# Optimization experiments

Hardware: AMD Instinct MI355X
Metric: run time of the kernel (lower is better)

The kernel has to match this reference:

```python
import jax, jax.numpy as jnp
import numpy as np
from jax import lax

CHUNK = 64
D_CONV = 4
EPS = 1e-5


def _rmsnorm(x, w):
    ms = jnp.mean(jnp.square(x.astype(jnp.float32)), axis=-1, keepdims=True)
    return x * lax.rsqrt(ms + EPS).astype(x.dtype) * w


def _conv_mix(x, proj_w, gate_w, conv_w, conv_b, out_proj_w):
    # x: [B,L,D] -> depthwise causal conv on projected channels, silu gate, out proj
    B, L, D = x.shape
    val = jnp.einsum('bld,ed->ble', x, proj_w)            # [B,L,d_inner]
    v = val.transpose(0, 2, 1)                            # [B,d_inner,L]
    d_inner = proj_w.shape[0]
    v = lax.conv_general_dilated(
        v, conv_w, window_strides=(1,), padding=[(D_CONV - 1, 0)],
        dimension_numbers=('NCH', 'OIH', 'NCH'), feature_group_count=d_inner)
    v = v + conv_b[None, :, None]
    val = jax.nn.silu(v.transpose(0, 2, 1))               # [B,L,d_inner]
    gate = jax.nn.silu(jnp.einsum('bld,ed->ble', x, gate_w))
    return jnp.einsum('ble,de->bld', val * gate, out_proj_w)


def _memory_attend(out, write_w, read_w, decay, log_alpha):
    B, T, D = out.shape
    C = CHUNK
    out32 = out.astype(jnp.float32)
    gamma = jax.nn.sigmoid(decay)
    log_gamma = jnp.log(gamma)
    v = jnp.einsum('btd,ed->bte', out32, write_w)         # proj_write
    wk = jnp.pad(out32[:, :-1], ((0, 0), (1, 0), (0, 0)))  # shifted keys
    rk = out32
    p = jnp.arange(C, dtype=jnp.float32)
    gp = gamma ** p                                       # [C]
    gw = gamma ** (C - 1 - p)                              # [C]
    diffs = jnp.maximum(p[:, None] - 1.0 - p[None, :], 0.0)
    M = jnp.exp(diffs * log_gamma) * (p[:, None] > p[None, :])  # [C,C]
    gC = gamma ** C
    Nc = T // C
    # scan axis first: [Nc,B,C,D]
    rk_c = rk.reshape(B, Nc, C, D).transpose(1, 0, 2, 3)
    wk_c = wk.reshape(B, Nc, C, D).transpose(1, 0, 2, 3)
    v_c = v.reshape(B, Nc, C, D).transpose(1, 0, 2, 3)

    def step(W, chunk):
        r, k, vv = chunk                                  # each [B,C,D]
        inter = jnp.einsum('bcd,bed->bce', r, W) * gp[None, :, None]
        S = jnp.einsum('bcd,bed->bce', r, k)              # [B,C,C]
        intra = jnp.einsum('bce,bed->bcd', S * M, vv)
        W_new = gC * W + jnp.einsum('bcd,bce->bde', vv * gw[None, :, None], k)
        return W_new, inter + intra

    W0 = jnp.zeros((B, D, D), dtype=jnp.float32)
    _, reads = lax.scan(step, W0, (rk_c, wk_c, v_c))      # [Nc,B,C,D]
    reads = reads.transpose(1, 0, 2, 3).reshape(B, T, D)
    read_out = jnp.einsum('btd,ed->bte', reads, read_w)
    return out + jnp.exp(log_alpha) * read_out.astype(out.dtype)


def setup_inputs() -> dict:
    key = jax.random.key(0)
    ks = jax.random.split(key, 9)
    B, T, D, d_inner = 8, 4096, 768, 1536
    s_d = 1.0 / np.sqrt(D)
    s_i = 1.0 / np.sqrt(d_inner)
    return {
        'x': jax.random.normal(ks[0], (B, T, D), jnp.float32),
        'norm_w': jnp.ones((D,), jnp.float32),
        'proj_w': jax.random.normal(ks[1], (d_inner, D), jnp.float32) * s_d,
        'gate_w': jax.random.normal(ks[2], (d_inner, D), jnp.float32) * s_d,
        'conv_w': jax.random.normal(ks[3], (d_inner, 1, D_CONV), jnp.float32) * 0.5,
        'conv_b': jnp.zeros((d_inner,), jnp.float32),
        'out_proj_w': jax.random.normal(ks[4], (D, d_inner), jnp.float32) * s_i,
        'write_w': jax.random.normal(ks[5], (D, D), jnp.float32) * s_d,
        'read_w': jax.random.normal(ks[6], (D, D), jnp.float32) * s_d,
        'decay': jnp.float32(4.6),
        'log_alpha': jnp.log(jnp.float32(0.03)),
    }


def reference(x, norm_w, proj_w, gate_w, conv_w, conv_b, out_proj_w, write_w, read_w, decay, log_alpha):
    out = _conv_mix(_rmsnorm(x, norm_w), proj_w, gate_w, conv_w, conv_b, out_proj_w)
    out = _memory_attend(out, write_w, read_w, decay, log_alpha)
    return x + out
```

## Files before the change

kernel.cpp:

```cpp
#include <hip/hip_runtime.h>
#include <stdint.h>


typedef short bf16s;
typedef __attribute__((ext_vector_type(8))) short short8;
typedef __attribute__((ext_vector_type(4))) float f32x4;

#define DEVINL __device__ __forceinline__

DEVINL float bf2f(short s) {
    union { unsigned u; float f; } v; v.u = ((unsigned)(unsigned short)s) << 16; return v.f;
}
DEVINL short f2bf(float f) {
    union { float f; unsigned u; } v; v.f = f;
    unsigned r = v.u + 0x7fffu + ((v.u >> 16) & 1u);
    return (short)(r >> 16);
}

DEVINL void glds16(void* lds, const void* g) {
    __builtin_amdgcn_global_load_lds(
        (const __attribute__((address_space(1))) void*)g,
        (__attribute__((address_space(3))) void*)lds, 16, 0, 0);
}

DEVINL void stage128(bf16s* lds, const bf16s* g, long gstride, int wave) {
#pragma unroll
    for (int p = 0; p < 4; ++p)
        glds16(lds + p * 2048 + wave * 512, g + (long)p * 32 * gstride);
}

DEVINL short8 fragr(const bf16s* t, int row, int kk, int q) {
    int f = kk * 4 + q;
    return *(const short8*)(t + row * 64 + ((f ^ (row & 7)) * 8));
}

#define MFMA(a, b, c) __builtin_amdgcn_mfma_f32_16x16x32_bf16((a), (b), (c), 0, 0, 0)

__global__ __launch_bounds__(256) void cast_w_kernel(
    const float* __restrict__ proj, const float* __restrict__ gate,
    const float* __restrict__ op, const float* __restrict__ wr, const float* __restrict__ rd,
    bf16s* __restrict__ w_pg, bf16s* __restrict__ w_op, bf16s* __restrict__ w_wr,
    bf16s* __restrict__ w_rd) {
    long i = (long)blockIdx.x * 256 + threadIdx.x;
    if (i < 1179648)        w_pg[i] = f2bf(proj[i]);
    else if (i < 2359296)   w_pg[i] = f2bf(gate[i - 1179648]);
    else if (i < 3538944)   w_op[i - 2359296] = f2bf(op[i - 2359296]);
    else if (i < 4128768)   w_wr[i - 3538944] = f2bf(wr[i - 3538944]);
    else if (i < 4718592)   w_rd[i - 4128768] = f2bf(rd[i - 4128768]);
}

__global__ __launch_bounds__(256) void rmsnorm_kernel(
    const float* __restrict__ x, const float* __restrict__ w, bf16s* __restrict__ xn) {
    long row = blockIdx.x;
    const float* xr = x + row * 768;
    int tid = threadIdx.x;
    float v0 = xr[tid], v1 = xr[tid + 256], v2 = xr[tid + 512];
    float ss = v0 * v0 + v1 * v1 + v2 * v2;
#pragma unroll
    for (int off = 32; off; off >>= 1) ss += __shfl_down(ss, off);
    __shared__ float p[4];
    if ((tid & 63) == 0) p[tid >> 6] = ss;
    __syncthreads();
    float tot = p[0] + p[1] + p[2] + p[3];
    float s = rsqrtf(tot * (1.0f / 768.0f) + 1e-5f);
    bf16s* o = xn + row * 768;
    o[tid]       = f2bf(v0 * s * w[tid]);
    o[tid + 256] = f2bf(v1 * s * w[tid + 256]);
    o[tid + 512] = f2bf(v2 * s * w[tid + 512]);
}

template <int MODE>
__global__ __launch_bounds__(256, 2) void gemm_kernel(
    const bf16s* __restrict__ A, const bf16s* __restrict__ B, int K, int N,
    bf16s* __restrict__ Cb, const float* __restrict__ xres,
    const bf16s* __restrict__ outres, const float* __restrict__ p_la,
    float* __restrict__ Cout) {
    __shared__ bf16s sA[128 * 64];
    __shared__ bf16s sB[128 * 64];
    const int tid = threadIdx.x;
    const int wave = tid >> 6, lane = tid & 63;
    const int wm = wave >> 1, wn = wave & 1;
    const int ln15 = lane & 15, q = lane >> 4;
    const long m0 = (long)blockIdx.y * 128, n0 = (long)blockIdx.x * 128;
    const int sr = tid >> 3;
    const int sf = (tid & 7) ^ (sr & 7);
    const bf16s* gA = A + (m0 + sr) * K + sf * 8;
    const bf16s* gB = B + (n0 + sr) * K + sf * 8;
    f32x4 acc[4][4] = {};
    const int nkt = K >> 6;
    for (int kt = 0; kt < nkt; ++kt) {
        __syncthreads();
        stage128(sA, gA, K, wave);
        stage128(sB, gB, K, wave);
        gA += 64; gB += 64;
        asm volatile("s_waitcnt vmcnt(0)" ::: "memory");
        __syncthreads();
#pragma unroll
        for (int kk = 0; kk < 2; ++kk) {
            short8 af[4], bf_[4];
#pragma unroll
            for (int i = 0; i < 4; ++i) af[i] = fragr(sA, wm * 64 + i * 16 + ln15, kk, q);
#pragma unroll
            for (int j = 0; j < 4; ++j) bf_[j] = fragr(sB, wn * 64 + j * 16 + ln15, kk, q);
#pragma unroll
            for (int i = 0; i < 4; ++i)
#pragma unroll
                for (int j = 0; j < 4; ++j) acc[i][j] = MFMA(af[i], bf_[j], acc[i][j]);
        }
    }
    float alpha = 0.f;
    if (MODE == 1) alpha = __expf(p_la[0]);
#pragma unroll
    for (int i = 0; i < 4; ++i)
#pragma unroll
        for (int j = 0; j < 4; ++j) {
            long mb = m0 + wm * 64 + i * 16 + q * 4;
            long nc = n0 + wn * 64 + j * 16 + ln15;
#pragma unroll
            for (int e = 0; e < 4; ++e) {
                long m = mb + e;
                float v = acc[i][j][e];
                if (MODE == 0) {
                    Cb[m * N + nc] = f2bf(v);
                } else {
                    long idx = m * 768 + nc;
                    Cout[idx] = xres[idx] + bf2f(outres[idx]) + alpha * v;
                }
            }
        }
}

__global__ __launch_bounds__(192) void conv_kernel(
    const bf16s* __restrict__ pg, const float* __restrict__ cw,
    const float* __restrict__ cb, bf16s* __restrict__ vg) {
    const int e0 = threadIdx.x * 8;
    const long l0 = (long)blockIdx.x * 16;
    float w0[8], w1[8], w2[8], w3[8], bias[8];
#pragma unroll
    for (int i = 0; i < 8; ++i) {
        const float* wc = cw + (e0 + i) * 4;
        w0[i] = wc[0]; w1[i] = wc[1]; w2[i] = wc[2]; w3[i] = wc[3];
        bias[i] = cb[e0 + i];
    }
    const bf16s* base = pg + l0 * 3072 + e0;
    short8 h0, h1, h2;
    if ((l0 & 4095) == 0) {
        short8 z = {0, 0, 0, 0, 0, 0, 0, 0};
        h0 = z; h1 = z; h2 = z;
    } else {
        h0 = *(const short8*)(base - 3 * 3072);
        h1 = *(const short8*)(base - 2 * 3072);
        h2 = *(const short8*)(base - 1 * 3072);
    }
    short8 cur = *(const short8*)base;
    short8 g8  = *(const short8*)(base + 1536);
    bf16s* out = vg + l0 * 1536 + e0;
#pragma unroll 4
    for (int t = 0; t < 16; ++t) {
        short8 ncur, ng;
        if (t < 15) {
            ncur = *(const short8*)(base + 3072);
            ng   = *(const short8*)(base + 3072 + 1536);
        }
        short8 o;
#pragma unroll
        for (int i = 0; i < 8; ++i) {
            float vv = bias[i] + bf2f(h0[i]) * w0[i] + bf2f(h1[i]) * w1[i]
                     + bf2f(h2[i]) * w2[i] + bf2f(cur[i]) * w3[i];
            float sv = vv / (1.0f + __expf(-vv));
            float gg = bf2f(g8[i]);
            o[i] = f2bf(sv * (gg / (1.0f + __expf(-gg))));
        }
        *(short8*)out = o;
        h0 = h1; h1 = h2; h2 = cur;
        cur = ncur; g8 = ng;
        base += 3072; out += 1536;
    }
}

template <int SHIFT, int GW>
__global__ __launch_bounds__(256) void transpose_kernel(
    const bf16s* __restrict__ src, bf16s* __restrict__ dst,
    const float* __restrict__ p_decay) {
    int b = blockIdx.z;
    long t0 = (long)blockIdx.y * 64, e0 = (long)blockIdx.x * 64;
    __shared__ bf16s tile[64][72];
    int tid = threadIdx.x;
    int r = tid >> 2, cs = (tid & 3) * 16;
    long tsrc = t0 + r - SHIFT;
    if (tsrc >= 0) {
        const bf16s* s = src + ((long)b * 4096 + tsrc) * 768 + e0 + cs;
        short8 v0 = *(const short8*)s;
        short8 v1 = *(const short8*)(s + 8);
        if (GW) {
            float gm = 1.0f / (1.0f + __expf(-p_decay[0]));
            float gwf = exp2f(__log2f(gm) * (float)(1023 - (int)(tsrc & 1023)));
#pragma unroll
            for (int i = 0; i < 8; ++i) {
                tile[r][cs + i]     = f2bf(bf2f(v0[i]) * gwf);
                tile[r][cs + 8 + i] = f2bf(bf2f(v1[i]) * gwf);
            }
        } else {
#pragma unroll
            for (int i = 0; i < 8; ++i) {
                tile[r][cs + i]     = v0[i];
                tile[r][cs + 8 + i] = v1[i];
            }
        }
    } else {
#pragma unroll
        for (int i = 0; i < 16; ++i) tile[r][cs + i] = 0;
    }
    __syncthreads();
    int er = tid >> 2, ts = (tid & 3) * 16;
    short8 a, bb;
#pragma unroll
    for (int i = 0; i < 8; ++i) a[i] = tile[ts + i][er];
#pragma unroll
    for (int i = 0; i < 8; ++i) bb[i] = tile[ts + 8 + i][er];
    bf16s* d = dst + ((long)b * 768 + e0 + er) * 4096 + t0 + ts;
    *(short8*)d = a;
    *(short8*)(d + 8) = bb;
}

__global__ __launch_bounds__(256, 2) void wstate_kernel(
    const bf16s* __restrict__ vTs, const bf16s* __restrict__ oTs,
    bf16s* __restrict__ Wst, const float* __restrict__ p_decay) {
    __shared__ bf16s sA[128 * 64];
    __shared__ bf16s sB[128 * 64];
    const int b = blockIdx.y;
    const int ti = blockIdx.x % 6, tj = blockIdx.x / 6;
    const int tid = threadIdx.x;
    const int wave = tid >> 6, lane = tid & 63;
    const int wm = wave >> 1, wn = wave & 1;
    const int ln15 = lane & 15, q = lane >> 4;
    const int sr = tid >> 3;
    const int sf = (tid & 7) ^ (sr & 7);
    const bf16s* gA = vTs + ((long)b * 768 + ti * 128 + sr) * 4096 + sf * 8;
    const bf16s* gB = oTs + ((long)b * 768 + tj * 128 + sr) * 4096 + sf * 8;
    const float gm = 1.0f / (1.0f + __expf(-p_decay[0]));
    const float gC = exp2f(__log2f(gm) * 1024.0f);
    f32x4 acc[4][4] = {};
    for (int jc = 0; jc < 4; ++jc) {
        bf16s* Wj = Wst + ((long)(b * 4 + jc)) * 768 * 768;
#pragma unroll
        for (int i = 0; i < 4; ++i)
#pragma unroll
            for (int jj = 0; jj < 4; ++jj) {
                long mb = ti * 128 + wm * 64 + i * 16 + q * 4;
                long nc = tj * 128 + wn * 64 + jj * 16 + ln15;
#pragma unroll
                for (int e = 0; e < 4; ++e) {
                    Wj[(mb + e) * 768 + nc] = f2bf(acc[i][jj][e]);
                    acc[i][jj][e] *= gC;
                }
            }
        for (int kt = 0; kt < 16; ++kt) {
            __syncthreads();
            stage128(sA, gA, 4096, wave);
            stage128(sB, gB, 4096, wave);
            gA += 64; gB += 64;
            asm volatile("s_waitcnt vmcnt(0)" ::: "memory");
            __syncthreads();
#pragma unroll
            for (int kk = 0; kk < 2; ++kk) {
                short8 af[4], bf_[4];
#pragma unroll
                for (int i = 0; i < 4; ++i) af[i] = fragr(sA, wm * 64 + i * 16 + ln15, kk, q);
#pragma unroll
                for (int j = 0; j < 4; ++j) bf_[j] = fragr(sB, wn * 64 + j * 16 + ln15, kk, q);
#pragma unroll
                for (int i = 0; i < 4; ++i)
#pragma unroll
                    for (int j = 0; j < 4; ++j) acc[i][j] = MFMA(af[i], bf_[j], acc[i][j]);
            }
        }
    }
}

__global__ __launch_bounds__(256, 2) void pmat_kernel(
    const bf16s* __restrict__ outb, bf16s* __restrict__ P,
    const float* __restrict__ p_decay) {
    const int ci = blockIdx.x >> 3, cj = blockIdx.x & 7;
    if (cj > ci) return;
    const int j = blockIdx.y, b = blockIdx.z;
    const bool fix = (j == 0 && cj == 0);
    __shared__ bf16s sA[128 * 64];
    __shared__ bf16s sB[128 * 64];
    const int tid = threadIdx.x;
    const int wave = tid >> 6, lane = tid & 63;
    const int wm = wave >> 1, wn = wave & 1;
    const int ln15 = lane & 15, q = lane >> 4;
    const int sr = tid >> 3;
    const int sf = (tid & 7) ^ (sr & 7);
    const bf16s* gA = outb + ((long)b * 4096 + j * 1024 + ci * 128 + sr) * 768 + sf * 8;
    const bf16s* gB = outb + ((long)b * 4096 + j * 1024 + cj * 128 + sr - 1) * 768 + sf * 8;
    f32x4 acc[4][4] = {};
    for (int kt = 0; kt < 12; ++kt) {
        __syncthreads();
        stage128(sA, gA, 768, wave);
        stage128(sB, gB, 768, wave);
        gA += 64; gB += 64;
        asm volatile("s_waitcnt vmcnt(0)" ::: "memory");
        __syncthreads();
        if (fix) {
            if (tid < 8) { short8 zz = {0,0,0,0,0,0,0,0}; ((short8*)sB)[tid] = zz; }
            __syncthreads();
        }
#pragma unroll
        for (int kk = 0; kk < 2; ++kk) {
            short8 af[4], bf_[4];
#pragma unroll
            for (int i = 0; i < 4; ++i) af[i] = fragr(sA, wm * 64 + i * 16 + ln15, kk, q);
#pragma unroll
            for (int jj = 0; jj < 4; ++jj) bf_[jj] = fragr(sB, wn * 64 + jj * 16 + ln15, kk, q);
#pragma unroll
            for (int i = 0; i < 4; ++i)
#pragma unroll
                for (int jj = 0; jj < 4; ++jj) acc[i][jj] = MFMA(af[i], bf_[jj], acc[i][jj]);
        }
    }
    const float lg = __log2f(1.0f / (1.0f + __expf(-p_decay[0])));
    bf16s* Pb = P + ((long)(b * 4 + j) << 20);
#pragma unroll
    for (int i = 0; i < 4; ++i)
#pragma unroll
        for (int jj = 0; jj < 4; ++jj) {
            int cb_ = ci * 128 + wm * 64 + i * 16 + q * 4;
            int cp  = cj * 128 + wn * 64 + jj * 16 + ln15;
#pragma unroll
            for (int e = 0; e < 4; ++e) {
                int c = cb_ + e;
                float val = (c > cp) ? acc[i][jj][e] * exp2f(lg * (float)(c - 1024)) : 0.0f;
                Pb[(long)c * 1024 + cp] = f2bf(val);
            }
        }
}

__global__ __launch_bounds__(256, 2) void reads_kernel(
    const bf16s* __restrict__ outb, const bf16s* __restrict__ Wst,
    const bf16s* __restrict__ Pm, const bf16s* __restrict__ vTs,
    bf16s* __restrict__ readsb, const float* __restrict__ p_decay) {
    const int ci = blockIdx.x & 7, vi = blockIdx.x >> 3;
    const int j = blockIdx.y, b = blockIdx.z;
    __shared__ bf16s sA[128 * 64];
    __shared__ bf16s sB[128 * 64];
    const int tid = threadIdx.x;
    const int wave = tid >> 6, lane = tid & 63;
    const int wm = wave >> 1, wn = wave & 1;
    const int ln15 = lane & 15, q = lane >> 4;
    const int sr = tid >> 3;
    const int sf = (tid & 7) ^ (sr & 7);
    const float lg = __log2f(1.0f / (1.0f + __expf(-p_decay[0])));
    f32x4 acc[4][4] = {};
    if (j > 0) {
        const bf16s* gA = outb + ((long)b * 4096 + j * 1024 + ci * 128 + sr) * 768 + sf * 8;
        const bf16s* gB = Wst + ((long)(b * 4 + j) * 768 + vi * 128 + sr) * 768 + sf * 8;
        for (int kt = 0; kt < 12; ++kt) {
            __syncthreads();
            stage128(sA, gA, 768, wave);
            stage128(sB, gB, 768, wave);
            gA += 64; gB += 64;
            asm volatile("s_waitcnt vmcnt(0)" ::: "memory");
            __syncthreads();
#pragma unroll
            for (int kk = 0; kk < 2; ++kk) {
                short8 af[4], bf_[4];
#pragma unroll
                for (int i = 0; i < 4; ++i) af[i] = fragr(sA, wm * 64 + i * 16 + ln15, kk, q);
#pragma unroll
                for (int jj = 0; jj < 4; ++jj) bf_[jj] = fragr(sB, wn * 64 + jj * 16 + ln15, kk, q);
#pragma unroll
                for (int i = 0; i < 4; ++i)
#pragma unroll
                    for (int jj = 0; jj < 4; ++jj) acc[i][jj] = MFMA(af[i], bf_[jj], acc[i][jj]);
            }
        }
#pragma unroll
        for (int i = 0; i < 4; ++i) {
            int cb_ = ci * 128 + wm * 64 + i * 16 + q * 4;
#pragma unroll
            for (int e = 0; e < 4; ++e) {
                float s = exp2f(lg * (float)(cb_ + e));
#pragma unroll
                for (int jj = 0; jj < 4; ++jj) acc[i][jj][e] *= s;
            }
        }
    }
    {
        const bf16s* gA = Pm + ((long)(b * 4 + j) << 20) + (long)(ci * 128 + sr) * 1024 + sf * 8;
        const bf16s* gB = vTs + ((long)b * 768 + vi * 128 + sr) * 4096 + j * 1024 + sf * 8;
        const int nkt = 2 * (ci + 1);
        for (int kt = 0; kt < nkt; ++kt) {
            __syncthreads();
            stage128(sA, gA, 1024, wave);
            stage128(sB, gB, 4096, wave);
            gA += 64; gB += 64;
            asm volatile("s_waitcnt vmcnt(0)" ::: "memory");
            __syncthreads();
#pragma unroll
            for (int kk = 0; kk < 2; ++kk) {
                short8 af[4], bf_[4];
#pragma unroll
                for (int i = 0; i < 4; ++i) af[i] = fragr(sA, wm * 64 + i * 16 + ln15, kk, q);
#pragma unroll
                for (int jj = 0; jj < 4; ++jj) bf_[jj] = fragr(sB, wn * 64 + jj * 16 + ln15, kk, q);
#pragma unroll
                for (int i = 0; i < 4; ++i)
#pragma unroll
                    for (int jj = 0; jj < 4; ++jj) acc[i][jj] = MFMA(af[i], bf_[jj], acc[i][jj]);
            }
        }
    }
#pragma unroll
    for (int i = 0; i < 4; ++i)
#pragma unroll
        for (int jj = 0; jj < 4; ++jj) {
            long tb = (long)j * 1024 + ci * 128 + wm * 64 + i * 16 + q * 4;
            long nc = vi * 128 + wn * 64 + jj * 16 + ln15;
#pragma unroll
            for (int e = 0; e < 4; ++e)
                readsb[((long)b * 4096 + tb + e) * 768 + nc] = f2bf(acc[i][jj][e]);
        }
}

extern "C" void kernel_launch(void* const* d_in, const int* in_sizes, int n_in,
                              void* d_out, int out_size, void* d_ws, size_t ws_size,
                              hipStream_t stream) {
    (void)in_sizes; (void)n_in; (void)out_size;
    const float* x      = (const float*)d_in[0];
    const float* norm_w = (const float*)d_in[1];
    const float* proj_w = (const float*)d_in[2];
    const float* gate_w = (const float*)d_in[3];
    const float* conv_w = (const float*)d_in[4];
    const float* conv_b = (const float*)d_in[5];
    const float* op_w   = (const float*)d_in[6];
    const float* wr_w   = (const float*)d_in[7];
    const float* rd_w   = (const float*)d_in[8];
    const float* decay  = (const float*)d_in[9];
    const float* la     = (const float*)d_in[10];

    char* ws = (char*)d_ws;
    size_t off = 0;
    auto alloc = [&](size_t bytes) { void* p = ws + off; off += (bytes + 255) & ~(size_t)255; return p; };
    bf16s* w_pg = (bf16s*)alloc(3072l * 768 * 2);
    bf16s* w_op = (bf16s*)alloc(768l * 1536 * 2);
    bf16s* w_wr = (bf16s*)alloc(768l * 768 * 2);
    bf16s* w_rd = (bf16s*)alloc(768l * 768 * 2);
    bf16s* RA   = (bf16s*)alloc(32768l * 768 * 2);
    bf16s* RB   = (bf16s*)alloc(2 * 32768l * 768 * 2);
    bf16s* RC   = (bf16s*)alloc(2 * 32768l * 768 * 2);
    bf16s* RE   = (bf16s*)alloc(32768l * 768 * 2);
    if (ws_size < off) return;

    bf16s* xn    = RA;
    bf16s* vTs   = RA;
    bf16s* pgH   = RB;
    bf16s* vb    = RB;
    bf16s* oTs   = RB + 25165824;
    bf16s* Pm    = RB;
    bf16s* vg    = RC;
    bf16s* Wst   = RC;
    bf16s* readsb= RC + 18874368;
    bf16s* outb  = RE;

    hipLaunchKernelGGL(cast_w_kernel, dim3(18432), dim3(256), 0, stream,
                       proj_w, gate_w, op_w, wr_w, rd_w, w_pg, w_op, w_wr, w_rd);
    hipLaunchKernelGGL(rmsnorm_kernel, dim3(32768), dim3(256), 0, stream, x, norm_w, xn);
    for (int h = 0; h < 2; ++h) {
        hipLaunchKernelGGL(HIP_KERNEL_NAME(gemm_kernel<0>), dim3(24, 128), dim3(256), 0, stream,
                           xn + (long)h * 16384 * 768, w_pg, 768, 3072, pgH,
                           (const float*)nullptr, (const bf16s*)nullptr, la, (float*)nullptr);
        hipLaunchKernelGGL(conv_kernel, dim3(1024), dim3(192), 0, stream,
                           pgH, conv_w, conv_b, vg + (long)h * 16384 * 1536);
    }
    hipLaunchKernelGGL(HIP_KERNEL_NAME(gemm_kernel<0>), dim3(6, 256), dim3(256), 0, stream,
                       vg, w_op, 1536, 768, outb,
                       (const float*)nullptr, (const bf16s*)nullptr, la, (float*)nullptr);
    hipLaunchKernelGGL(HIP_KERNEL_NAME(gemm_kernel<0>), dim3(6, 256), dim3(256), 0, stream,
                       outb, w_wr, 768, 768, vb,
                       (const float*)nullptr, (const bf16s*)nullptr, la, (float*)nullptr);
    hipLaunchKernelGGL(HIP_KERNEL_NAME(transpose_kernel<1, 0>), dim3(12, 64, 8), dim3(256), 0, stream,
                       outb, oTs, decay);
    hipLaunchKernelGGL(HIP_KERNEL_NAME(transpose_kernel<0, 1>), dim3(12, 64, 8), dim3(256), 0, stream,
                       vb, vTs, decay);
    hipLaunchKernelGGL(wstate_kernel, dim3(36, 8), dim3(256), 0, stream,
                       vTs, oTs, Wst, decay);
    hipLaunchKernelGGL(pmat_kernel, dim3(64, 4, 8), dim3(256), 0, stream,
                       outb, Pm, decay);
    hipLaunchKernelGGL(reads_kernel, dim3(48, 4, 8), dim3(256), 0, stream,
                       outb, Wst, Pm, vTs, readsb, decay);
    hipLaunchKernelGGL(HIP_KERNEL_NAME(gemm_kernel<1>), dim3(6, 256), dim3(256), 0, stream,
                       readsb, w_rd, 768, 768, (bf16s*)nullptr,
                       x, outb, la, (float*)d_out);
}
```

Measured before the change: 971.8 us.

## Double-buffer LDS staging in all GEMMs, parallelize state computation and compact pmat grid

All MFMA GEMM kernels now stage the next K-tile into a second LDS buffer while computing on the current one, using partial vmcnt waits to overlap global loads with MFMA work. The sequential per-chunk wstate kernel is split into a parallel ugemm kernel computing each chunk's update independently, followed by a small wcombine kernel that applies the decay recurrence. The pmat grid launches only lower-triangular tiles instead of early-exiting half the blocks, and reads_kernel prefetches the second GEMM's first tile during the first GEMM's last step. Doubled LDS (64KB per block) may reduce occupancy, and the bf16 rounding of intermediate chunk states in the combine step changes numerics slightly.

```diff
diff --git a/kernel.cpp b/kernel.cpp
--- a/kernel.cpp
+++ b/kernel.cpp
@@ -22,6 +22,8 @@
         (const __attribute__((address_space(1))) void*)g,
         (__attribute__((address_space(3))) void*)lds, 16, 0, 0);
 }
+DEVINL void wait_vm8() { asm volatile("s_waitcnt vmcnt(8)" ::: "memory"); }
+DEVINL void wait_vm0() { asm volatile("s_waitcnt vmcnt(0)" ::: "memory"); }
 
 DEVINL void stage128(bf16s* lds, const bf16s* g, long gstride, int wave) {
 #pragma unroll
@@ -35,6 +37,22 @@
 }
 
 #define MFMA(a, b, c) __builtin_amdgcn_mfma_f32_16x16x32_bf16((a), (b), (c), 0, 0, 0)
+
+DEVINL void comp44(const bf16s* cA, const bf16s* cB, f32x4 (&acc)[4][4],
+                   int wm, int wn, int ln15, int q) {
+#pragma unroll
+    for (int kk = 0; kk < 2; ++kk) {
+        short8 af[4], bf_[4];
+#pragma unroll
+        for (int i = 0; i < 4; ++i) af[i] = fragr(cA, wm * 64 + i * 16 + ln15, kk, q);
+#pragma unroll
+        for (int j = 0; j < 4; ++j) bf_[j] = fragr(cB, wn * 64 + j * 16 + ln15, kk, q);
+#pragma unroll
+        for (int i = 0; i < 4; ++i)
+#pragma unroll
+            for (int j = 0; j < 4; ++j) acc[i][j] = MFMA(af[i], bf_[j], acc[i][j]);
+    }
+}
 
 __global__ __launch_bounds__(256) void cast_w_kernel(
     const float* __restrict__ proj, const float* __restrict__ gate,
@@ -75,8 +93,8 @@
     bf16s* __restrict__ Cb, const float* __restrict__ xres,
     const bf16s* __restrict__ outres, const float* __restrict__ p_la,
     float* __restrict__ Cout) {
-    __shared__ bf16s sA[128 * 64];
-    __shared__ bf16s sB[128 * 64];
+    __shared__ bf16s sA[2][8192];
+    __shared__ bf16s sB[2][8192];
     const int tid = threadIdx.x;
     const int wave = tid >> 6, lane = tid & 63;
     const int wm = wave >> 1, wn = wave & 1;
@@ -86,30 +104,27 @@
     const int sf = (tid & 7) ^ (sr & 7);
     const bf16s* gA = A + (m0 + sr) * K + sf * 8;
     const bf16s* gB = B + (n0 + sr) * K + sf * 8;
+    float alpha = 0.f;
+    if (MODE == 1) alpha = __expf(p_la[0]);
+    wait_vm0();
     f32x4 acc[4][4] = {};
     const int nkt = K >> 6;
+    stage128(sA[0], gA, K, wave);
+    stage128(sB[0], gB, K, wave);
+    gA += 64; gB += 64;
     for (int kt = 0; kt < nkt; ++kt) {
-        __syncthreads();
-        stage128(sA, gA, K, wave);
-        stage128(sB, gB, K, wave);
-        gA += 64; gB += 64;
-        asm volatile("s_waitcnt vmcnt(0)" ::: "memory");
-        __syncthreads();
-#pragma unroll
-        for (int kk = 0; kk < 2; ++kk) {
-            short8 af[4], bf_[4];
-#pragma unroll
-            for (int i = 0; i < 4; ++i) af[i] = fragr(sA, wm * 64 + i * 16 + ln15, kk, q);
-#pragma unroll
-            for (int j = 0; j < 4; ++j) bf_[j] = fragr(sB, wn * 64 + j * 16 + ln15, kk, q);
-#pragma unroll
-            for (int i = 0; i < 4; ++i)
-#pragma unroll
-                for (int j = 0; j < 4; ++j) acc[i][j] = MFMA(af[i], bf_[j], acc[i][j]);
-        }
-    }
-    float alpha = 0.f;
-    if (MODE == 1) alpha = __expf(p_la[0]);
+        const bf16s* cA = sA[kt & 1];
+        const bf16s* cB = sB[kt & 1];
+        if (kt + 1 < nkt) {
+            stage128(sA[(kt + 1) & 1], gA, K, wave);
+            stage128(sB[(kt + 1) & 1], gB, K, wave);
+            gA += 64; gB += 64;
+            wait_vm8();
+        } else wait_vm0();
+        __syncthreads();
+        comp44(cA, cB, acc, wm, wn, ln15, q);
+        __syncthreads();
+    }
 #pragma unroll
     for (int i = 0; i < 4; ++i)
 #pragma unroll
@@ -223,12 +238,12 @@
     *(short8*)(d + 8) = bb;
 }
 
-__global__ __launch_bounds__(256, 2) void wstate_kernel(
+__global__ __launch_bounds__(256, 2) void ugemm_kernel(
     const bf16s* __restrict__ vTs, const bf16s* __restrict__ oTs,
-    bf16s* __restrict__ Wst, const float* __restrict__ p_decay) {
-    __shared__ bf16s sA[128 * 64];
-    __shared__ bf16s sB[128 * 64];
-    const int b = blockIdx.y;
+    bf16s* __restrict__ Wst) {
+    __shared__ bf16s sA[2][8192];
+    __shared__ bf16s sB[2][8192];
+    const int b = blockIdx.z, jc = blockIdx.y;
     const int ti = blockIdx.x % 6, tj = blockIdx.x / 6;
     const int tid = threadIdx.x;
     const int wave = tid >> 6, lane = tid & 63;
@@ -236,115 +251,72 @@
     const int ln15 = lane & 15, q = lane >> 4;
     const int sr = tid >> 3;
     const int sf = (tid & 7) ^ (sr & 7);
-    const bf16s* gA = vTs + ((long)b * 768 + ti * 128 + sr) * 4096 + sf * 8;
-    const bf16s* gB = oTs + ((long)b * 768 + tj * 128 + sr) * 4096 + sf * 8;
+    const bf16s* gA = vTs + ((long)b * 768 + ti * 128 + sr) * 4096 + jc * 1024 + sf * 8;
+    const bf16s* gB = oTs + ((long)b * 768 + tj * 128 + sr) * 4096 + jc * 1024 + sf * 8;
+    f32x4 acc[4][4] = {};
+    stage128(sA[0], gA, 4096, wave);
+    stage128(sB[0], gB, 4096, wave);
+    gA += 64; gB += 64;
+    for (int kt = 0; kt < 16; ++kt) {
+        const bf16s* cA = sA[kt & 1];
+        const bf16s* cB = sB[kt & 1];
+        if (kt + 1 < 16) {
+            stage128(sA[(kt + 1) & 1], gA, 4096, wave);
+            stage128(sB[(kt + 1) & 1], gB, 4096, wave);
+            gA += 64; gB += 64;
+            wait_vm8();
+        } else wait_vm0();
+        __syncthreads();
+        comp44(cA, cB, acc, wm, wn, ln15, q);
+        __syncthreads();
+    }
+    bf16s* Wj = Wst + (long)(b * 4 + jc) * 589824;
+#pragma unroll
+    for (int i = 0; i < 4; ++i)
+#pragma unroll
+        for (int jj = 0; jj < 4; ++jj) {
+            long mb = ti * 128 + wm * 64 + i * 16 + q * 4;
+            long nc = tj * 128 + wn * 64 + jj * 16 + ln15;
+#pragma unroll
+            for (int e = 0; e < 4; ++e)
+                Wj[(mb + e) * 768 + nc] = f2bf(acc[i][jj][e]);
+        }
+}
+
+__global__ __launch_bounds__(256) void wcombine_kernel(
+    bf16s* __restrict__ Wst, const float* __restrict__ p_decay) {
+    const int b = blockIdx.y;
+    const long o = ((long)blockIdx.x * 256 + threadIdx.x) * 8;
     const float gm = 1.0f / (1.0f + __expf(-p_decay[0]));
     const float gC = exp2f(__log2f(gm) * 1024.0f);
-    f32x4 acc[4][4] = {};
-    for (int jc = 0; jc < 4; ++jc) {
-        bf16s* Wj = Wst + ((long)(b * 4 + jc)) * 768 * 768;
-#pragma unroll
-        for (int i = 0; i < 4; ++i)
-#pragma unroll
-            for (int jj = 0; jj < 4; ++jj) {
-                long mb = ti * 128 + wm * 64 + i * 16 + q * 4;
-                long nc = tj * 128 + wn * 64 + jj * 16 + ln15;
-#pragma unroll
-                for (int e = 0; e < 4; ++e) {
-                    Wj[(mb + e) * 768 + nc] = f2bf(acc[i][jj][e]);
-                    acc[i][jj][e] *= gC;
-                }
-            }
-        for (int kt = 0; kt < 16; ++kt) {
-            __syncthreads();
-            stage128(sA, gA, 4096, wave);
-            stage128(sB, gB, 4096, wave);
-            gA += 64; gB += 64;
-            asm volatile("s_waitcnt vmcnt(0)" ::: "memory");
-            __syncthreads();
-#pragma unroll
-            for (int kk = 0; kk < 2; ++kk) {
-                short8 af[4], bf_[4];
-#pragma unroll
-                for (int i = 0; i < 4; ++i) af[i] = fragr(sA, wm * 64 + i * 16 + ln15, kk, q);
-#pragma unroll
-                for (int j = 0; j < 4; ++j) bf_[j] = fragr(sB, wn * 64 + j * 16 + ln15, kk, q);
-#pragma unroll
-                for (int i = 0; i < 4; ++i)
-#pragma unroll
-                    for (int j = 0; j < 4; ++j) acc[i][j] = MFMA(af[i], bf_[j], acc[i][j]);
-            }
-        }
-    }
+    bf16s* s0 = Wst + (long)(b * 4 + 0) * 589824 + o;
+    bf16s* s1 = Wst + (long)(b * 4 + 1) * 589824 + o;
+    bf16s* s2 = Wst + (long)(b * 4 + 2) * 589824 + o;
+    bf16s* s3 = Wst + (long)(b * 4 + 3) * 589824 + o;
+    short8 u0 = *(short8*)s0, u1 = *(short8*)s1, u2 = *(short8*)s2;
+    short8 w2, w3, z = {0, 0, 0, 0, 0, 0, 0, 0};
+#pragma unroll
+    for (int i = 0; i < 8; ++i) {
+        float f0 = bf2f(u0[i]), f1 = bf2f(u1[i]), f2 = bf2f(u2[i]);
+        w2[i] = f2bf(gC * f0 + f1);
+        w3[i] = f2bf(gC * (gC * f0 + f1) + f2);
+    }
+    *(short8*)s3 = w3;
+    *(short8*)s2 = w2;
+    *(short8*)s1 = u0;
+    *(short8*)s0 = z;
 }
 
 __global__ __launch_bounds__(256, 2) void pmat_kernel(
     const bf16s* __restrict__ outb, bf16s* __restrict__ P,
     const float* __restrict__ p_decay) {
-    const int ci = blockIdx.x >> 3, cj = blockIdx.x & 7;
-    if (cj > ci) return;
+    int rem = blockIdx.x, ci = 0;
+    while (rem >= ci + 1) { rem -= ci + 1; ci++; }
+    const int cj = rem;
     const int j = blockIdx.y, b = blockIdx.z;
     const bool fix = (j == 0 && cj == 0);
-    __shared__ bf16s sA[128 * 64];
-    __shared__ bf16s sB[128 * 64];
-    const int tid = threadIdx.x;
-    const int wave = tid >> 6, lane = tid & 63;
-    const int wm = wave >> 1, wn = wave & 1;
-    const int ln15 = lane & 15, q = lane >> 4;
-    const int sr = tid >> 3;
-    const int sf = (tid & 7) ^ (sr & 7);
-    const bf16s* gA = outb + ((long)b * 4096 + j * 1024 + ci * 128 + sr) * 768 + sf * 8;
-    const bf16s* gB = outb + ((long)b * 4096 + j * 1024 + cj * 128 + sr - 1) * 768 + sf * 8;
-    f32x4 acc[4][4] = {};
-    for (int kt = 0; kt < 12; ++kt) {
-        __syncthreads();
-        stage128(sA, gA, 768, wave);
-        stage128(sB, gB, 768, wave);
-        gA += 64; gB += 64;
-        asm volatile("s_waitcnt vmcnt(0)" ::: "memory");
-        __syncthreads();
-        if (fix) {
-            if (tid < 8) { short8 zz = {0,0,0,0,0,0,0,0}; ((short8*)sB)[tid] = zz; }
-            __syncthreads();
-        }
-#pragma unroll
-        for (int kk = 0; kk < 2; ++kk) {
-            short8 af[4], bf_[4];
-#pragma unroll
-            for (int i = 0; i < 4; ++i) af[i] = fragr(sA, wm * 64 + i * 16 + ln15, kk, q);
-#pragma unroll
-            for (int jj = 0; jj < 4; ++jj) bf_[jj] = fragr(sB, wn * 64 + jj * 16 + ln15, kk, q);
-#pragma unroll
-            for (int i = 0; i < 4; ++i)
-#pragma unroll
-                for (int jj = 0; jj < 4; ++jj) acc[i][jj] = MFMA(af[i], bf_[jj], acc[i][jj]);
-        }
-    }
-    const float lg = __log2f(1.0f / (1.0f + __expf(-p_decay[0])));
-    bf16s* Pb = P + ((long)(b * 4 + j) << 20);
-#pragma unroll
-    for (int i = 0; i < 4; ++i)
-#pragma unroll
-        for (int jj = 0; jj < 4; ++jj) {
-            int cb_ = ci * 128 + wm * 64 + i * 16 + q * 4;
-            int cp  = cj * 128 + wn * 64 + jj * 16 + ln15;
-#pragma unroll
-            for (int e = 0; e < 4; ++e) {
-                int c = cb_ + e;
-                float val = (c > cp) ? acc[i][jj][e] * exp2f(lg * (float)(c - 1024)) : 0.0f;
-                Pb[(long)c * 1024 + cp] = f2bf(val);
-            }
-        }
-}
-
-__global__ __launch_bounds__(256, 2) void reads_kernel(
-    const bf16s* __restrict__ outb, const bf16s* __restrict__ Wst,
-    const bf16s* __restrict__ Pm, const bf16s* __restrict__ vTs,
-    bf16s* __restrict__ readsb, const float* __restrict__ p_decay) {
-    const int ci = blockIdx.x & 7, vi = blockIdx.x >> 3;
-    const int j = blockIdx.y, b = blockIdx.z;
-    __shared__ bf16s sA[128 * 64];
-    __shared__ bf16s sB[128 * 64];
+    __shared__ bf16s sA[2][8192];
+    __shared__ bf16s sB[2][8192];
     const int tid = threadIdx.x;
     const int wave = tid >> 6, lane = tid & 63;
     const int wm = wave >> 1, wn = wave & 1;
@@ -352,29 +324,87 @@
     const int sr = tid >> 3;
     const int sf = (tid & 7) ^ (sr & 7);
     const float lg = __log2f(1.0f / (1.0f + __expf(-p_decay[0])));
+    wait_vm0();
+    const bf16s* gA = outb + ((long)b * 4096 + j * 1024 + ci * 128 + sr) * 768 + sf * 8;
+    const bf16s* gB = outb + ((long)b * 4096 + j * 1024 + cj * 128 + sr - 1) * 768 + sf * 8;
+    f32x4 acc[4][4] = {};
+    stage128(sA[0], gA, 768, wave);
+    stage128(sB[0], gB, 768, wave);
+    gA += 64; gB += 64;
+    for (int kt = 0; kt < 12; ++kt) {
+        const bf16s* cA = sA[kt & 1];
+        bf16s* cB = sB[kt & 1];
+        if (kt + 1 < 12) {
+            stage128(sA[(kt + 1) & 1], gA, 768, wave);
+            stage128(sB[(kt + 1) & 1], gB, 768, wave);
+            gA += 64; gB += 64;
+            wait_vm8();
+        } else wait_vm0();
+        __syncthreads();
+        if (fix) {
+            if (tid < 8) { short8 zz = {0,0,0,0,0,0,0,0}; ((short8*)cB)[tid] = zz; }
+            __syncthreads();
+        }
+        comp44(cA, cB, acc, wm, wn, ln15, q);
+        __syncthreads();
+    }
+    bf16s* Pb = P + ((long)(b * 4 + j) << 20);
+#pragma unroll
+    for (int i = 0; i < 4; ++i)
+#pragma unroll
+        for (int jj = 0; jj < 4; ++jj) {
+            int cb_ = ci * 128 + wm * 64 + i * 16 + q * 4;
+            int cp  = cj * 128 + wn * 64 + jj * 16 + ln15;
+#pragma unroll
+            for (int e = 0; e < 4; ++e) {
+                int c = cb_ + e;
+                float val = (c > cp) ? acc[i][jj][e] * exp2f(lg * (float)(c - 1024)) : 0.0f;
+                Pb[(long)c * 1024 + cp] = f2bf(val);
+            }
+        }
+}
+
+__global__ __launch_bounds__(256, 2) void reads_kernel(
+    const bf16s* __restrict__ outb, const bf16s* __restrict__ Wst,
+    const bf16s* __restrict__ Pm, const bf16s* __restrict__ vTs,
+    bf16s* __restrict__ readsb, const float* __restrict__ p_decay) {
+    const int ci = blockIdx.x & 7, vi = blockIdx.x >> 3;
+    const int j = blockIdx.y, b = blockIdx.z;
+    __shared__ bf16s sA[2][8192];
+    __shared__ bf16s sB[2][8192];
+    const int tid = threadIdx.x;
+    const int wave = tid >> 6, lane = tid & 63;
+    const int wm = wave >> 1, wn = wave & 1;
+    const int ln15 = lane & 15, q = lane >> 4;
+    const int sr = tid >> 3;
+    const int sf = (tid & 7) ^ (sr & 7);
+    const float lg = __log2f(1.0f / (1.0f + __expf(-p_decay[0])));
+    wait_vm0();
+    const bf16s* gA2 = Pm + ((long)(b * 4 + j) << 20) + (long)(ci * 128 + sr) * 1024 + sf * 8;
+    const bf16s* gB2 = vTs + ((long)b * 768 + vi * 128 + sr) * 4096 + j * 1024 + sf * 8;
     f32x4 acc[4][4] = {};
     if (j > 0) {
         const bf16s* gA = outb + ((long)b * 4096 + j * 1024 + ci * 128 + sr) * 768 + sf * 8;
         const bf16s* gB = Wst + ((long)(b * 4 + j) * 768 + vi * 128 + sr) * 768 + sf * 8;
+        stage128(sA[0], gA, 768, wave);
+        stage128(sB[0], gB, 768, wave);
+        gA += 64; gB += 64;
         for (int kt = 0; kt < 12; ++kt) {
+            const bf16s* cA = sA[kt & 1];
+            const bf16s* cB = sB[kt & 1];
+            if (kt + 1 < 12) {
+                stage128(sA[(kt + 1) & 1], gA, 768, wave);
+                stage128(sB[(kt + 1) & 1], gB, 768, wave);
+                gA += 64; gB += 64;
+            } else {
+                stage128(sA[0], gA2, 1024, wave);
+                stage128(sB[0], gB2, 4096, wave);
+                gA2 += 64; gB2 += 64;
+            }
+            wait_vm8();
             __syncthreads();
-            stage128(sA, gA, 768, wave);
-            stage128(sB, gB, 768, wave);
-            gA += 64; gB += 64;
-            asm volatile("s_waitcnt vmcnt(0)" ::: "memory");
+            comp44(cA, cB, acc, wm, wn, ln15, q);
             __syncthreads();
-#pragma unroll
-            for (int kk = 0; kk < 2; ++kk) {
-                short8 af[4], bf_[4];
-#pragma unroll
-                for (int i = 0; i < 4; ++i) af[i] = fragr(sA, wm * 64 + i * 16 + ln15, kk, q);
-#pragma unroll
-                for (int jj = 0; jj < 4; ++jj) bf_[jj] = fragr(sB, wn * 64 + jj * 16 + ln15, kk, q);
-#pragma unroll
-                for (int i = 0; i < 4; ++i)
-#pragma unroll
-                    for (int jj = 0; jj < 4; ++jj) acc[i][jj] = MFMA(af[i], bf_[jj], acc[i][jj]);
-            }
         }
 #pragma unroll
         for (int i = 0; i < 4; ++i) {
@@ -386,31 +416,24 @@
                 for (int jj = 0; jj < 4; ++jj) acc[i][jj][e] *= s;
             }
         }
-    }
-    {
-        const bf16s* gA = Pm + ((long)(b * 4 + j) << 20) + (long)(ci * 128 + sr) * 1024 + sf * 8;
-        const bf16s* gB = vTs + ((long)b * 768 + vi * 128 + sr) * 4096 + j * 1024 + sf * 8;
-        const int nkt = 2 * (ci + 1);
-        for (int kt = 0; kt < nkt; ++kt) {
-            __syncthreads();
-            stage128(sA, gA, 1024, wave);
-            stage128(sB, gB, 4096, wave);
-            gA += 64; gB += 64;
-            asm volatile("s_waitcnt vmcnt(0)" ::: "memory");
-            __syncthreads();
-#pragma unroll
-            for (int kk = 0; kk < 2; ++kk) {
-                short8 af[4], bf_[4];
-#pragma unroll
-                for (int i = 0; i < 4; ++i) af[i] = fragr(sA, wm * 64 + i * 16 + ln15, kk, q);
-#pragma unroll
-                for (int jj = 0; jj < 4; ++jj) bf_[jj] = fragr(sB, wn * 64 + jj * 16 + ln15, kk, q);
-#pragma unroll
-                for (int i = 0; i < 4; ++i)
-#pragma unroll
-                    for (int jj = 0; jj < 4; ++jj) acc[i][jj] = MFMA(af[i], bf_[jj], acc[i][jj]);
-            }
-        }
+    } else {
+        stage128(sA[0], gA2, 1024, wave);
+        stage128(sB[0], gB2, 4096, wave);
+        gA2 += 64; gB2 += 64;
+    }
+    const int nkt2 = 2 * (ci + 1);
+    for (int kt = 0; kt < nkt2; ++kt) {
+        const bf16s* cA = sA[kt & 1];
+        const bf16s* cB = sB[kt & 1];
+        if (kt + 1 < nkt2) {
+            stage128(sA[(kt + 1) & 1], gA2, 1024, wave);
+            stage128(sB[(kt + 1) & 1], gB2, 4096, wave);
+            gA2 += 64; gB2 += 64;
+            wait_vm8();
+        } else wait_vm0();
+        __syncthreads();
+        comp44(cA, cB, acc, wm, wn, ln15, q);
+        __syncthreads();
     }
 #pragma unroll
     for (int i = 0; i < 4; ++i)
@@ -484,9 +507,11 @@
                        outb, oTs, decay);
     hipLaunchKernelGGL(HIP_KERNEL_NAME(transpose_kernel<0, 1>), dim3(12, 64, 8), dim3(256), 0, stream,
                        vb, vTs, decay);
-    hipLaunchKernelGGL(wstate_kernel, dim3(36, 8), dim3(256), 0, stream,
-                       vTs, oTs, Wst, decay);
-    hipLaunchKernelGGL(pmat_kernel, dim3(64, 4, 8), dim3(256), 0, stream,
+    hipLaunchKernelGGL(ugemm_kernel, dim3(36, 4, 8), dim3(256), 0, stream,
+                       vTs, oTs, Wst);
+    hipLaunchKernelGGL(wcombine_kernel, dim3(288, 8), dim3(256), 0, stream,
+                       Wst, decay);
+    hipLaunchKernelGGL(pmat_kernel, dim3(36, 4, 8), dim3(256), 0, stream,
                        outb, Pm, decay);
     hipLaunchKernelGGL(reads_kernel, dim3(48, 4, 8), dim3(256), 0, stream,
                        outb, Wst, Pm, vTs, readsb, decay);
```

After: 1.044 ms. 7.4% more time.
